# Kernel optimization log

Measured on AMD Instinct MI355X. Metric: run time of the kernel, lower is better.

## Reference

```python
import jax, jax.numpy as jnp
import numpy as np
from jax import lax

V, D, L = 32000, 1024, 8
HQ, HKV, HD = 16, 4, 64          # head_dim = D // HQ
H = int(2.6875 * D)              # SwiGLU hidden = 2752
B, S = 2, 1024
WINDOW, GEVERY = 256, 4
EPS, BASE = 1e-6, 10000.0
STD = 0.02


def setup_inputs() -> dict:
    key = jax.random.key(0)
    ks = jax.random.split(key, 10)
    return {
        "idx": jax.random.randint(ks[0], (B, S), 0, V, dtype=jnp.int32),
        "emb": jax.random.normal(ks[1], (V, D), jnp.float32) * STD,
        "Wq": jax.random.normal(ks[2], (L, D, HQ * HD), jnp.float32) * STD,
        "Wk": jax.random.normal(ks[3], (L, D, HKV * HD), jnp.float32) * STD,
        "Wv": jax.random.normal(ks[4], (L, D, HKV * HD), jnp.float32) * STD,
        "Wo": jax.random.normal(ks[5], (L, HQ * HD, D), jnp.float32) * (STD / np.sqrt(2 * L)).astype(np.float32),
        "w1": jax.random.normal(ks[6], (L, D, H), jnp.float32) * STD,
        "w3": jax.random.normal(ks[7], (L, D, H), jnp.float32) * STD,
        "w2": jax.random.normal(ks[8], (L, H, D), jnp.float32) * (STD / np.sqrt(2 * L)).astype(np.float32),
        "n1": jnp.ones((L, D), jnp.float32),
        "n2": jnp.ones((L, D), jnp.float32),
        "nf": jnp.ones((D,), jnp.float32),
    }


def _rmsnorm(x, w):
    return x * lax.rsqrt(jnp.mean(x * x, axis=-1, keepdims=True) + EPS) * w


def _rope(x, cos, sin):
    # x: [B,S,h,HD]; pairs (even, odd) rotated by complex multiply with e^{i*theta}
    x2 = x.reshape(*x.shape[:-1], HD // 2, 2)
    x0, x1 = x2[..., 0], x2[..., 1]
    r0 = x0 * cos - x1 * sin
    r1 = x0 * sin + x1 * cos
    return jnp.stack([r0, r1], axis=-1).reshape(x.shape)


def _forward(idx, emb, Wq, Wk, Wv, Wo, w1, w3, w2, n1, n2, nf):
    # RoPE cache (RoPECache._build_cache)
    inv_freq = 1.0 / (BASE ** (jnp.arange(0, HD, 2, dtype=jnp.float32) / HD))
    t = jnp.arange(S, dtype=jnp.float32)
    freqs = t[:, None] * inv_freq[None, :]                      # [S, HD//2]
    cos = jnp.cos(freqs)[None, :, None, :]                      # [1,S,1,HD//2]
    sin = jnp.sin(freqs)[None, :, None, :]

    # masks: global causal and sliding-window causal (additive, 0 / -inf)
    pos = jnp.arange(S)
    causal = pos[None, :] <= pos[:, None]
    local = causal & ((pos[:, None] - pos[None, :]) < WINDOW)
    neg_inf = jnp.float32(-jnp.inf)
    gmask = jnp.where(causal, 0.0, neg_inf).astype(jnp.float32)
    lmask = jnp.where(local, 0.0, neg_inf).astype(jnp.float32)
    use_global = ((jnp.arange(L) + 1) % GEVERY) == 0            # [L] bool

    scale = 1.0 / (HD ** 0.5)
    rep = HQ // HKV

    def block(x, p):
        wq, wk, wv, wo, W1, W3, W2, g1, g2, ug = p
        h = _rmsnorm(x, g1)
        q = (h @ wq).reshape(B, S, HQ, HD)
        k = (h @ wk).reshape(B, S, HKV, HD)
        v = (h @ wv).reshape(B, S, HKV, HD)
        q = _rope(q, cos, sin)
        k = _rope(k, cos, sin)
        k = jnp.repeat(k, rep, axis=2)                          # GQA: expand KV heads
        v = jnp.repeat(v, rep, axis=2)
        mask = jnp.where(ug, gmask, lmask)
        sc = jnp.einsum('bqhd,bkhd->bhqk', q, k) * scale + mask
        attn = jax.nn.softmax(sc, axis=-1)
        o = jnp.einsum('bhqk,bkhd->bqhd', attn, v).reshape(B, S, HQ * HD)
        x = x + o @ wo
        h2 = _rmsnorm(x, g2)
        x = x + (jax.nn.silu(h2 @ W1) * (h2 @ W3)) @ W2
        return x, None

    x = emb[idx]                                                # token embedding
    x, _ = lax.scan(block, x, (Wq, Wk, Wv, Wo, w1, w3, w2, n1, n2, use_global))
    logits = _rmsnorm(x, nf) @ emb.T                            # tied lm_head
    return logits


def reference(idx, emb, Wq, Wk, Wv, Wo, w1, w3, w2, n1, n2, nf):
    return _forward(idx, emb, Wq, Wk, Wv, Wo, w1, w3, w2, n1, n2, nf)
```

## Files before the change

### kernel.cpp

```cpp
#include <hip/hip_runtime.h>

#define V_ 32000
#define D_ 1024
#define L_ 8
#define HQ_ 16
#define HKV_ 4
#define HD_ 64
#define H_ 2752
#define B_ 2
#define S_ 1024
#define BS_ 2048
#define WINDOW_ 256

typedef float f32x4 __attribute__((ext_vector_type(4)));
typedef short s16x8 __attribute__((ext_vector_type(8)));
typedef unsigned short u16;

__device__ __forceinline__ u16 f2b(float f) {
  union { float f; unsigned u; } a; a.f = f;
  return (u16)((a.u + 0x7fffu + ((a.u >> 16) & 1u)) >> 16);
}
__device__ __forceinline__ float b2f(u16 b) {
  union { unsigned u; float f; } a; a.u = ((unsigned)b) << 16; return a.f;
}

__device__ __forceinline__ void gload_lds16(const void* g, void* l) {
  __builtin_amdgcn_global_load_lds(
      (const __attribute__((address_space(1))) void*)(unsigned long long)(uintptr_t)g,
      (__attribute__((address_space(3))) void*)(unsigned int)(uintptr_t)l,
      16, 0, 0);
}

__global__ void k_cvt(const float* __restrict__ src, u16* __restrict__ dst, long n4) {
  long i = (long)blockIdx.x * blockDim.x + threadIdx.x;
  if (i >= n4) return;
  float4 v = ((const float4*)src)[i];
  ushort4 o; o.x = f2b(v.x); o.y = f2b(v.y); o.z = f2b(v.z); o.w = f2b(v.w);
  ((ushort4*)dst)[i] = o;
}

struct TMat { const float* src; u16* dst; int R, C, t0, mul, add; };
struct T7 { TMat m[7]; };

__global__ void k_transpose7(T7 P) {
  __shared__ float tile[32][33];
  int bid = blockIdx.x;
  int mi = 0;
#pragma unroll
  for (int i = 1; i < 7; ++i) if (bid >= P.m[i].t0) mi = i;
  TMat mm = P.m[mi];
  int tl = bid - mm.t0;
  int ct = mm.C >> 5;
  int tr = tl / ct, tc = tl - tr * ct;
  int r0 = tr << 5, c0 = tc << 5;
  int tx = threadIdx.x & 31, ty = threadIdx.x >> 5;
#pragma unroll
  for (int j = 0; j < 4; ++j)
    tile[ty + j * 8][tx] = mm.src[(size_t)(r0 + ty + j * 8) * mm.C + c0 + tx];
  __syncthreads();
#pragma unroll
  for (int j = 0; j < 4; ++j)
    mm.dst[((size_t)(c0 + ty + j * 8) * mm.mul + mm.add) * mm.R + r0 + tx] =
        f2b(tile[tx][ty + j * 8]);
}

__global__ void k_embed(const int* __restrict__ idx, const float* __restrict__ emb,
                        float* __restrict__ x) {
  int t = blockIdx.x;
  int token = idx[t];
  const float4* s = (const float4*)(emb + (size_t)token * D_);
  float4* d = (float4*)(x + (size_t)t * D_);
  d[threadIdx.x] = s[threadIdx.x];
}

__global__ void k_rmsnorm(const float* __restrict__ x, const float* __restrict__ w,
                          u16* __restrict__ out) {
  int row = blockIdx.x, tid = threadIdx.x;
  float4 v = ((const float4*)(x + (size_t)row * D_))[tid];
  float ss = v.x * v.x + v.y * v.y + v.z * v.z + v.w * v.w;
#pragma unroll
  for (int m = 1; m < 64; m <<= 1) ss += __shfl_xor(ss, m, 64);
  __shared__ float red[4];
  if ((tid & 63) == 0) red[tid >> 6] = ss;
  __syncthreads();
  float tot = red[0] + red[1] + red[2] + red[3];
  float rs = rsqrtf(tot * (1.0f / D_) + 1e-6f);
  float4 wv = ((const float4*)w)[tid];
  ushort4 o;
  o.x = f2b(v.x * rs * wv.x); o.y = f2b(v.y * rs * wv.y);
  o.z = f2b(v.z * rs * wv.z); o.w = f2b(v.w * rs * wv.w);
  ((ushort4*)(out + (size_t)row * D_))[tid] = o;
}

__global__ void k_ropetab(float* __restrict__ cosT, float* __restrict__ sinT) {
  int i = blockIdx.x * blockDim.x + threadIdx.x;
  int s = i >> 5, d = i & 31;
  float inv = __expf(-((float)(2 * d) / (float)HD_) * logf(10000.0f));
  float f = (float)s * inv;
  cosT[i] = cosf(f); sinT[i] = sinf(f);
}

__global__ void k_ropev(const float* __restrict__ qkvf, const float* __restrict__ cosT,
                        const float* __restrict__ sinT, u16* __restrict__ qh,
                        u16* __restrict__ kh, u16* __restrict__ vth) {
  __shared__ float tile[32][65];
  int bid = blockIdx.x;
  int tid = threadIdx.x;
  if (bid < BS_) {
    int t = bid;
    int b = t >> 10, s = t & (S_ - 1);
    const float* row = qkvf + (size_t)t * 1536;
    for (int p = tid; p < 512; p += 256) {
      int hh = p >> 5, d = p & 31;
      float x0 = row[hh * 64 + 2 * d], x1 = row[hh * 64 + 2 * d + 1];
      float c = cosT[s * 32 + d], sn = sinT[s * 32 + d];
      size_t o = ((size_t)(b * HQ_ + hh) * S_ + s) * HD_ + 2 * d;
      qh[o] = f2b(x0 * c - x1 * sn);
      qh[o + 1] = f2b(x0 * sn + x1 * c);
    }
    if (tid < 128) {
      int hh = tid >> 5, d = tid & 31;
      float x0 = row[1024 + hh * 64 + 2 * d], x1 = row[1024 + hh * 64 + 2 * d + 1];
      float c = cosT[s * 32 + d], sn = sinT[s * 32 + d];
      size_t o = ((size_t)(b * HKV_ + hh) * S_ + s) * HD_ + 2 * d;
      kh[o] = f2b(x0 * c - x1 * sn);
      kh[o + 1] = f2b(x0 * sn + x1 * c);
    }
  } else {
    int v = bid - BS_;
    const int s0 = (v & 31) << 5, hh = (v >> 5) & 3, b = v >> 7;
    const int tx = tid & 63, ty = tid >> 6;
#pragma unroll
    for (int j = 0; j < 8; ++j) {
      int sl = j * 4 + ty;
      tile[sl][tx] = qkvf[(size_t)((b << 10) + s0 + sl) * 1536 + 1280 + hh * 64 + tx];
    }
    __syncthreads();
    const int sx = tid & 31, dr = tid >> 5;
#pragma unroll
    for (int j = 0; j < 8; ++j) {
      int d = j * 8 + dr;
      vth[((size_t)((b * HKV_ + hh) << 6) + d) * S_ + s0 + sx] = f2b(tile[sx][d]);
    }
  }
}

template <int EPI>
__global__ __launch_bounds__(256) void k_gemm(const u16* __restrict__ A,
                                              const u16* __restrict__ BT,
                                              void* __restrict__ Cp, int kdepth,
                                              int lda, int ldc) {
  __shared__ u16 As[3][4096];
  __shared__ u16 Bs[3][4096];
  const int tid = threadIdx.x;
  const int lane = tid & 63, wid = tid >> 6;
  const int lin = blockIdx.y * 16 + blockIdx.x;
  const int cpx = (gridDim.x * gridDim.y) >> 3;
  const int swz = (lin & 7) * cpx + (lin >> 3);
  const int m0 = (swz & 15) << 7, n0 = (swz >> 4) << 7;
  const int wm = (wid >> 1) << 6, wn = (wid & 1) << 6;
  const int fr = lane & 15, fg = lane >> 4;

  f32x4 acc[4][4] = {};

  const int srow = (wid << 4) + (lane >> 2);
  const int scol = ((lane & 3) - ((lane >> 3) & 3)) & 3;
  const int kz = blockIdx.z * kdepth;
  const u16* ga = A + (size_t)(m0 + srow) * lda + kz + (scol << 3);
  const u16* gb = BT + (size_t)(n0 + srow) * lda + kz + (scol << 3);
  const int cb = wid << 9;

  auto stage = [&](int buf, int k0) {
    u16* la = &As[buf][cb];
    u16* lb = &Bs[buf][cb];
    gload_lds16(ga + k0, la);
    gload_lds16(ga + (size_t)64 * lda + k0, la + 2048);
    gload_lds16(gb + k0, lb);
    gload_lds16(gb + (size_t)64 * lda + k0, lb + 2048);
  };

  const int nk = kdepth >> 5;
  stage(0, 0);
  stage(1, 32);

  const int ab = (wid >> 1) << 2, bb = (wid & 1) << 2;
  const int foff = (fr << 5) + ((((fg + (fr >> 1)) & 3)) << 3);
  int cur = 0;
  for (int t = 0; t < nk; ++t) {
    if (t + 2 < nk) {
      int nb = cur + 2; if (nb >= 3) nb -= 3;
      stage(nb, (t + 2) << 5);
      asm volatile("s_waitcnt vmcnt(8)" ::: "memory");
    } else if (t + 2 == nk) {
      asm volatile("s_waitcnt vmcnt(4)" ::: "memory");
    } else {
      asm volatile("s_waitcnt vmcnt(0)" ::: "memory");
    }
    __builtin_amdgcn_s_barrier();
    s16x8 af[4], bq[4];
#pragma unroll
    for (int i = 0; i < 4; ++i) {
      af[i] = *(const s16x8*)(&As[cur][((ab + i) << 9) + foff]);
      bq[i] = *(const s16x8*)(&Bs[cur][((bb + i) << 9) + foff]);
    }
#pragma unroll
    for (int mi = 0; mi < 4; ++mi)
#pragma unroll
      for (int ni = 0; ni < 4; ++ni)
        acc[mi][ni] = __builtin_amdgcn_mfma_f32_16x16x32_bf16(af[mi], bq[ni], acc[mi][ni], 0, 0, 0);
    __builtin_amdgcn_s_barrier();
    if (++cur == 3) cur = 0;
  }

#pragma unroll
  for (int mi = 0; mi < 4; ++mi) {
#pragma unroll
    for (int ni = 0; ni < 4; ++ni) {
#pragma unroll
      for (int r = 0; r < 4; ++r) {
        int row = m0 + wm + mi * 16 + fg * 4 + r;
        int col = n0 + wn + ni * 16 + fr;
        size_t off = (size_t)row * ldc + col;
        float v = acc[mi][ni][r];
        if (EPI == 0) ((float*)Cp)[off] = v;
        else atomicAdd((float*)Cp + off, v);
      }
    }
  }
}

template <int EPI>
__global__ __launch_bounds__(512, 4) void k_gemm2(const u16* __restrict__ A,
                                                  const u16* __restrict__ BT,
                                                  void* __restrict__ Cp, int K, int ldc) {
  __shared__ u16 As[3][8192];
  __shared__ u16 Bs[3][4096];
  const int tid = threadIdx.x;
  const int lane = tid & 63, wid = tid >> 6;
  const int lin = blockIdx.y * gridDim.x + blockIdx.x;
  const int cpx = (gridDim.x * gridDim.y) >> 3;
  const int swz = (lin & 7) * cpx + (lin >> 3);
  const int m0 = (swz & 7) << 8, n0 = (swz >> 3) << 7;
  const int fr = lane & 15, fg = lane >> 4;

  f32x4 acc[4][4] = {};

  const int srow = lane >> 2;
  const int scol = ((lane & 3) - ((lane >> 3) & 3)) & 3;
  const u16* ga = A + (size_t)(m0 + (wid << 5) + srow) * K + (scol << 3);
  const u16* gb = BT + (size_t)(n0 + (wid << 4) + srow) * K + (scol << 3);
  const int cba = wid << 10;
  const int cbb = wid << 9;

  auto stage = [&](int buf, int k0) {
    gload_lds16(ga + k0, &As[buf][cba]);
    gload_lds16(ga + (size_t)16 * K + k0, &As[buf][cba + 512]);
    gload_lds16(gb + k0, &Bs[buf][cbb]);
  };

  const int nk = K >> 5;
  stage(0, 0);
  stage(1, 32);

  const int am = (wid >> 1) << 2;
  const int bn = (wid & 1) << 2;
  const int foff = (fr << 5) + ((((fg + (fr >> 1)) & 3)) << 3);
  int cur = 0;
  for (int t = 0; t < nk; ++t) {
    if (t + 2 < nk) {
      int nb = cur + 2; if (nb >= 3) nb -= 3;
      stage(nb, (t + 2) << 5);
      asm volatile("s_waitcnt vmcnt(6)" ::: "memory");
    } else if (t + 2 == nk) {
      asm volatile("s_waitcnt vmcnt(3)" ::: "memory");
    } else {
      asm volatile("s_waitcnt vmcnt(0)" ::: "memory");
    }
    __builtin_amdgcn_s_barrier();
    s16x8 af[4], bq[4];
#pragma unroll
    for (int i = 0; i < 4; ++i) {
      af[i] = *(const s16x8*)(&As[cur][((am + i) << 9) + foff]);
      bq[i] = *(const s16x8*)(&Bs[cur][((bn + i) << 9) + foff]);
    }
#pragma unroll
    for (int mi = 0; mi < 4; ++mi)
#pragma unroll
      for (int ni = 0; ni < 4; ++ni)
        acc[mi][ni] = __builtin_amdgcn_mfma_f32_16x16x32_bf16(af[mi], bq[ni], acc[mi][ni], 0, 0, 0);
    __builtin_amdgcn_s_barrier();
    if (++cur == 3) cur = 0;
  }

#pragma unroll
  for (int mi = 0; mi < 4; ++mi) {
#pragma unroll
    for (int ni = 0; ni < 4; ++ni) {
#pragma unroll
      for (int r = 0; r < 4; ++r) {
        int row = m0 + ((wid >> 1) << 6) + mi * 16 + fg * 4 + r;
        int col = n0 + ((wid & 1) << 6) + ni * 16 + fr;
        float v = acc[mi][ni][r];
        if (EPI == 0) {
          ((float*)Cp)[(size_t)row * ldc + col] = v;
        } else {
          float o = __shfl_xor(v, 1, 64);
          if (!(fr & 1)) {
            float s = v / (1.0f + __expf(-v)) * o;
            ((u16*)Cp)[(size_t)row * ldc + (col >> 1)] = f2b(s);
          }
        }
      }
    }
  }
}

__global__ __launch_bounds__(256) void k_attn(const u16* __restrict__ qh,
                                              const u16* __restrict__ kh,
                                              const u16* __restrict__ vth,
                                              u16* __restrict__ attno, int isGlobal) {
  __shared__ u16 pb[4][512];
  const int qblk = blockIdx.x, hq = blockIdx.y, b = blockIdx.z;
  const int lane = threadIdx.x & 63, wid = threadIdx.x >> 6;
  const int fr = lane & 15, fg = lane >> 4;
  const int q0 = (qblk << 6) + (wid << 4);
  const int hk = hq >> 2;
  const u16* Q = qh + ((size_t)(b * HQ_ + hq) * S_) * HD_;
  const u16* Kh = kh + ((size_t)(b * HKV_ + hk) * S_) * HD_;
  const u16* VT = vth + ((size_t)(b * HKV_ + hk) * HD_) * S_;
  u16* pbuf = pb[wid];

  const s16x8 aq0 = *(const s16x8*)(Q + (q0 + fr) * HD_ + fg * 8);
  const s16x8 aq1 = *(const s16x8*)(Q + (q0 + fr) * HD_ + 32 + fg * 8);

  f32x4 o0 = {}, o1 = {}, o2 = {}, o3 = {};
  float m[4], l[4];
#pragma unroll
  for (int r = 0; r < 4; ++r) { m[r] = -1e30f; l[r] = 0.0f; }

  int kt0 = 0;
  if (!isGlobal) { int lo = q0 - (WINDOW_ - 1); if (lo > 0) kt0 = lo & ~31; }
  const int ktend = q0 + 16;

  for (int kt = kt0; kt < ktend; kt += 32) {
    f32x4 sc0 = {}, sc1 = {};
    {
      s16x8 b0 = *(const s16x8*)(Kh + (kt + fr) * HD_ + fg * 8);
      s16x8 b1 = *(const s16x8*)(Kh + (kt + fr) * HD_ + 32 + fg * 8);
      sc0 = __builtin_amdgcn_mfma_f32_16x16x32_bf16(aq0, b0, sc0, 0, 0, 0);
      sc0 = __builtin_amdgcn_mfma_f32_16x16x32_bf16(aq1, b1, sc0, 0, 0, 0);
      s16x8 c0 = *(const s16x8*)(Kh + (kt + 16 + fr) * HD_ + fg * 8);
      s16x8 c1 = *(const s16x8*)(Kh + (kt + 16 + fr) * HD_ + 32 + fg * 8);
      sc1 = __builtin_amdgcn_mfma_f32_16x16x32_bf16(aq0, c0, sc1, 0, 0, 0);
      sc1 = __builtin_amdgcn_mfma_f32_16x16x32_bf16(aq1, c1, sc1, 0, 0, 0);
    }
#pragma unroll
    for (int r = 0; r < 4; ++r) {
      int row = q0 + fg * 4 + r;
      int col0 = kt + fr, col1 = kt + 16 + fr;
      bool v0 = (col0 <= row) && (isGlobal || (row - col0) < WINDOW_);
      bool v1 = (col1 <= row) && (isGlobal || (row - col1) < WINDOW_);
      float s0 = v0 ? sc0[r] * 0.125f : -1e30f;
      float s1 = v1 ? sc1[r] * 0.125f : -1e30f;
      float t = fmaxf(s0, s1);
#pragma unroll
      for (int msk = 1; msk < 16; msk <<= 1) t = fmaxf(t, __shfl_xor(t, msk, 16));
      float mn = fmaxf(m[r], t);
      float fsc = __expf(m[r] - mn);
      m[r] = mn;
      float p0 = v0 ? __expf(s0 - mn) : 0.0f;
      float p1 = v1 ? __expf(s1 - mn) : 0.0f;
      float ps = p0 + p1;
#pragma unroll
      for (int msk = 1; msk < 16; msk <<= 1) ps += __shfl_xor(ps, msk, 16);
      l[r] = l[r] * fsc + ps;
      o0[r] *= fsc; o1[r] *= fsc; o2[r] *= fsc; o3[r] *= fsc;
      pbuf[(fg * 4 + r) * 32 + fr] = f2b(p0);
      pbuf[(fg * 4 + r) * 32 + 16 + fr] = f2b(p1);
    }
    s16x8 ap = *(const s16x8*)(pbuf + fr * 32 + fg * 8);
    {
      s16x8 bv0 = *(const s16x8*)(VT + (size_t)(0 + fr) * S_ + kt + fg * 8);
      o0 = __builtin_amdgcn_mfma_f32_16x16x32_bf16(ap, bv0, o0, 0, 0, 0);
      s16x8 bv1 = *(const s16x8*)(VT + (size_t)(16 + fr) * S_ + kt + fg * 8);
      o1 = __builtin_amdgcn_mfma_f32_16x16x32_bf16(ap, bv1, o1, 0, 0, 0);
      s16x8 bv2 = *(const s16x8*)(VT + (size_t)(32 + fr) * S_ + kt + fg * 8);
      o2 = __builtin_amdgcn_mfma_f32_16x16x32_bf16(ap, bv2, o2, 0, 0, 0);
      s16x8 bv3 = *(const s16x8*)(VT + (size_t)(48 + fr) * S_ + kt + fg * 8);
      o3 = __builtin_amdgcn_mfma_f32_16x16x32_bf16(ap, bv3, o3, 0, 0, 0);
    }
  }

#pragma unroll
  for (int r = 0; r < 4; ++r) {
    int row = q0 + fg * 4 + r;
    float inv = 1.0f / l[r];
    size_t base = ((size_t)b * S_ + row) * (HQ_ * HD_) + hq * HD_;
    attno[base + fr] = f2b(o0[r] * inv);
    attno[base + 16 + fr] = f2b(o1[r] * inv);
    attno[base + 32 + fr] = f2b(o2[r] * inv);
    attno[base + 48 + fr] = f2b(o3[r] * inv);
  }
}

extern "C" void kernel_launch(void* const* d_in, const int* in_sizes, int n_in,
                              void* d_out, int out_size, void* d_ws, size_t ws_size,
                              hipStream_t stream) {
  (void)in_sizes; (void)n_in; (void)out_size; (void)ws_size;
  const int* idx = (const int*)d_in[0];
  const float* emb = (const float*)d_in[1];
  const float* Wq = (const float*)d_in[2];
  const float* Wk = (const float*)d_in[3];
  const float* Wv = (const float*)d_in[4];
  const float* Wo = (const float*)d_in[5];
  const float* w1 = (const float*)d_in[6];
  const float* w3 = (const float*)d_in[7];
  const float* w2 = (const float*)d_in[8];
  const float* n1 = (const float*)d_in[9];
  const float* n2 = (const float*)d_in[10];
  const float* nf = (const float*)d_in[11];
  float* out = (float*)d_out;

  char* p = (char*)d_ws;
  auto carve = [&](size_t bytes) {
    char* q = p;
    p += (bytes + 255) & ~(size_t)255;
    return (void*)q;
  };
  float* x = (float*)carve((size_t)BS_ * D_ * 4);
  u16* h = (u16*)carve((size_t)BS_ * D_ * 2);
  float* qkvf = (float*)carve((size_t)BS_ * 1536 * 4);
  u16* qh = (u16*)carve((size_t)B_ * HQ_ * S_ * HD_ * 2);
  u16* khb = (u16*)carve((size_t)B_ * HKV_ * S_ * HD_ * 2);
  u16* vth = (u16*)carve((size_t)B_ * HKV_ * HD_ * S_ * 2);
  u16* attno = (u16*)carve((size_t)BS_ * D_ * 2);
  u16* g = (u16*)carve((size_t)BS_ * H_ * 2);
  u16* wT = (u16*)carve((size_t)11075584 * 2);
  float* cosT = (float*)carve((size_t)S_ * 32 * 4);
  float* sinT = (float*)carve((size_t)S_ * 32 * 4);
  u16* embb = (u16*)carve((size_t)V_ * D_ * 2);

  k_cvt<<<V_ * D_ / 4 / 256, 256, 0, stream>>>(emb, embb, (long)V_ * D_ / 4);
  k_ropetab<<<S_ * 32 / 256, 256, 0, stream>>>(cosT, sinT);
  k_embed<<<BS_, 256, 0, stream>>>(idx, emb, x);

  for (int l = 0; l < L_; ++l) {
    T7 t7;
    t7.m[0] = { Wq + (size_t)l * D_ * 1024, wT, D_, 1024, 0, 1, 0 };
    t7.m[1] = { Wk + (size_t)l * D_ * 256, wT + 1048576, D_, 256, 1024, 1, 0 };
    t7.m[2] = { Wv + (size_t)l * D_ * 256, wT + 1310720, D_, 256, 1280, 1, 0 };
    t7.m[3] = { Wo + (size_t)l * 1024 * D_, wT + 1572864, 1024, D_, 1536, 1, 0 };
    t7.m[4] = { w1 + (size_t)l * D_ * H_, wT + 2621440, D_, H_, 2560, 2, 0 };
    t7.m[5] = { w3 + (size_t)l * D_ * H_, wT + 2621440, D_, H_, 5312, 2, 1 };
    t7.m[6] = { w2 + (size_t)l * H_ * D_, wT + 8257536, H_, D_, 8064, 1, 0 };
    k_transpose7<<<10816, 256, 0, stream>>>(t7);

    k_rmsnorm<<<BS_, 256, 0, stream>>>(x, n1 + (size_t)l * D_, h);
    k_gemm<0><<<dim3(16, 12), 256, 0, stream>>>(h, wT, qkvf, 1024, 1024, 1536);
    k_ropev<<<BS_ + 256, 256, 0, stream>>>(qkvf, cosT, sinT, qh, khb, vth);
    int ig = ((l + 1) % 4) == 0;
    k_attn<<<dim3(16, HQ_, B_), 256, 0, stream>>>(qh, khb, vth, attno, ig);
    k_gemm<4><<<dim3(16, 8, 2), 256, 0, stream>>>(attno, wT + 1572864, x, 512, 1024, 1024);
    k_rmsnorm<<<BS_, 256, 0, stream>>>(x, n2 + (size_t)l * D_, h);
    k_gemm2<3><<<dim3(8, 43), 512, 0, stream>>>(h, wT + 2621440, g, 1024, 2752);
    k_gemm<4><<<dim3(16, 8, 2), 256, 0, stream>>>(g, wT + 8257536, x, 1376, 2752, 1024);
  }

  k_rmsnorm<<<BS_, 256, 0, stream>>>(x, nf, h);
  k_gemm2<0><<<dim3(8, 250), 512, 0, stream>>>(h, embb, out, 1024, 32000);
}
```

Measured before the change: 1.496 ms.

## Use 4-stage LDS ring with two K-steps per barrier in large GEMM

Turns the big GEMM kernel's triple-buffered LDS pipeline into a 4-buffer ring. Each iteration now prefetches and computes two K-slices, so there is one barrier pair per two K-steps instead of per step. It also raises wave priority around the MFMA blocks with s_setprio. The costs are more shared memory per block (96KB vs 72KB), which can reduce blocks per CU, and dropping the min-occupancy launch bound. The pipeline also assumes nk is even.

```diff
diff --git a/kernel.cpp b/kernel.cpp
--- a/kernel.cpp
+++ b/kernel.cpp
@@ -230,11 +230,11 @@
 }
 
 template <int EPI>
-__global__ __launch_bounds__(512, 4) void k_gemm2(const u16* __restrict__ A,
-                                                  const u16* __restrict__ BT,
-                                                  void* __restrict__ Cp, int K, int ldc) {
-  __shared__ u16 As[3][8192];
-  __shared__ u16 Bs[3][4096];
+__global__ __launch_bounds__(512) void k_gemm8(const u16* __restrict__ A,
+                                               const u16* __restrict__ BT,
+                                               void* __restrict__ Cp, int K, int ldc) {
+  __shared__ u16 As[4][8192];
+  __shared__ u16 Bs[4][4096];
   const int tid = threadIdx.x;
   const int lane = tid & 63, wid = tid >> 6;
   const int lin = blockIdx.y * gridDim.x + blockIdx.x;
@@ -265,31 +265,49 @@
   const int am = (wid >> 1) << 2;
   const int bn = (wid & 1) << 2;
   const int foff = (fr << 5) + ((((fg + (fr >> 1)) & 3)) << 3);
-  int cur = 0;
-  for (int t = 0; t < nk; ++t) {
-    if (t + 2 < nk) {
-      int nb = cur + 2; if (nb >= 3) nb -= 3;
-      stage(nb, (t + 2) << 5);
+  for (int j = 0; j < (nk >> 1); ++j) {
+    const int t0 = j << 1;
+    const int c0 = t0 & 3, c1 = (t0 + 1) & 3;
+    if (t0 + 2 < nk) {
+      stage((t0 + 2) & 3, (t0 + 2) << 5);
+      stage((t0 + 3) & 3, (t0 + 3) << 5);
       asm volatile("s_waitcnt vmcnt(6)" ::: "memory");
-    } else if (t + 2 == nk) {
-      asm volatile("s_waitcnt vmcnt(3)" ::: "memory");
     } else {
       asm volatile("s_waitcnt vmcnt(0)" ::: "memory");
     }
     __builtin_amdgcn_s_barrier();
-    s16x8 af[4], bq[4];
-#pragma unroll
-    for (int i = 0; i < 4; ++i) {
-      af[i] = *(const s16x8*)(&As[cur][((am + i) << 9) + foff]);
-      bq[i] = *(const s16x8*)(&Bs[cur][((bn + i) << 9) + foff]);
-    }
-#pragma unroll
-    for (int mi = 0; mi < 4; ++mi)
-#pragma unroll
-      for (int ni = 0; ni < 4; ++ni)
-        acc[mi][ni] = __builtin_amdgcn_mfma_f32_16x16x32_bf16(af[mi], bq[ni], acc[mi][ni], 0, 0, 0);
+    {
+      s16x8 af[4], bq[4];
+#pragma unroll
+      for (int i = 0; i < 4; ++i) {
+        af[i] = *(const s16x8*)(&As[c0][((am + i) << 9) + foff]);
+        bq[i] = *(const s16x8*)(&Bs[c0][((bn + i) << 9) + foff]);
+      }
+      __builtin_amdgcn_s_setprio(1);
+#pragma unroll
+      for (int mi = 0; mi < 4; ++mi)
+#pragma unroll
+        for (int ni = 0; ni < 4; ++ni)
+          acc[mi][ni] = __builtin_amdgcn_mfma_f32_16x16x32_bf16(af[mi], bq[ni], acc[mi][ni], 0, 0, 0);
+      __builtin_amdgcn_s_setprio(0);
+    }
+    {
+      s16x8 af[4], bq[4];
+#pragma unroll
+      for (int i = 0; i < 4; ++i) {
+        af[i] = *(const s16x8*)(&As[c1][((am + i) << 9) + foff]);
+        bq[i] = *(const s16x8*)(&Bs[c1][((bn + i) << 9) + foff]);
+      }
+      __builtin_amdgcn_s_setprio(1);
+#pragma unroll
+      for (int mi = 0; mi < 4; ++mi)
+#pragma unroll
+        for (int ni = 0; ni < 4; ++ni)
+          acc[mi][ni] = __builtin_amdgcn_mfma_f32_16x16x32_bf16(af[mi], bq[ni], acc[mi][ni], 0, 0, 0);
+      __builtin_amdgcn_s_setprio(0);
+    }
+    asm volatile("" ::: "memory");
     __builtin_amdgcn_s_barrier();
-    if (++cur == 3) cur = 0;
   }
 
 #pragma unroll
@@ -462,10 +480,10 @@
     k_attn<<<dim3(16, HQ_, B_), 256, 0, stream>>>(qh, khb, vth, attno, ig);
     k_gemm<4><<<dim3(16, 8, 2), 256, 0, stream>>>(attno, wT + 1572864, x, 512, 1024, 1024);
     k_rmsnorm<<<BS_, 256, 0, stream>>>(x, n2 + (size_t)l * D_, h);
-    k_gemm2<3><<<dim3(8, 43), 512, 0, stream>>>(h, wT + 2621440, g, 1024, 2752);
+    k_gemm8<3><<<dim3(8, 43), 512, 0, stream>>>(h, wT + 2621440, g, 1024, 2752);
     k_gemm<4><<<dim3(16, 8, 2), 256, 0, stream>>>(g, wT + 8257536, x, 1376, 2752, 1024);
   }
 
   k_rmsnorm<<<BS_, 256, 0, stream>>>(x, nf, h);
-  k_gemm2<0><<<dim3(8, 250), 512, 0, stream>>>(h, embb, out, 1024, 32000);
-}
+  k_gemm8<0><<<dim3(8, 250), 512, 0, stream>>>(h, embb, out, 1024, 32000);
+}
```

Result: slower. 1.667 ms (+11.5%).

## Fuse RoPE into QKV GEMM epilogue and merge init kernels

Applied to the files above, without the earlier changes.

Applies the rotary embedding to Q and K directly in the QKV GEMM epilogue, using a lane shuffle to fetch the paired even/odd element and writing bf16 head-major outputs. Only V is still written as fp32 and transposed by a slimmed kernel. The bf16 embedding conversion and RoPE table kernels are merged into one launch. This removes the fp32 round trip of Q/K through global memory and a few launches, at the cost of scattered 2-byte stores and table loads in the GEMM epilogue.

```diff
diff --git a/kernel.cpp b/kernel.cpp
--- a/kernel.cpp
+++ b/kernel.cpp
@@ -31,12 +31,21 @@
       16, 0, 0);
 }
 
-__global__ void k_cvt(const float* __restrict__ src, u16* __restrict__ dst, long n4) {
-  long i = (long)blockIdx.x * blockDim.x + threadIdx.x;
-  if (i >= n4) return;
-  float4 v = ((const float4*)src)[i];
-  ushort4 o; o.x = f2b(v.x); o.y = f2b(v.y); o.z = f2b(v.z); o.w = f2b(v.w);
-  ((ushort4*)dst)[i] = o;
+__global__ void k_init(const float* __restrict__ src, u16* __restrict__ dst,
+                       float* __restrict__ cosT, float* __restrict__ sinT) {
+  int bid = blockIdx.x;
+  if (bid < 32000) {
+    long i = (long)bid * 256 + threadIdx.x;
+    float4 v = ((const float4*)src)[i];
+    ushort4 o; o.x = f2b(v.x); o.y = f2b(v.y); o.z = f2b(v.z); o.w = f2b(v.w);
+    ((ushort4*)dst)[i] = o;
+  } else {
+    int i = (bid - 32000) * 256 + threadIdx.x;
+    int s = i >> 5, d = i & 31;
+    float inv = __expf(-((float)(2 * d) / (float)HD_) * logf(10000.0f));
+    float f = (float)s * inv;
+    cosT[i] = cosf(f); sinT[i] = sinf(f);
+  }
 }
 
 struct TMat { const float* src; u16* dst; int R, C, t0, mul, add; };
@@ -92,56 +101,21 @@
   ((ushort4*)(out + (size_t)row * D_))[tid] = o;
 }
 
-__global__ void k_ropetab(float* __restrict__ cosT, float* __restrict__ sinT) {
-  int i = blockIdx.x * blockDim.x + threadIdx.x;
-  int s = i >> 5, d = i & 31;
-  float inv = __expf(-((float)(2 * d) / (float)HD_) * logf(10000.0f));
-  float f = (float)s * inv;
-  cosT[i] = cosf(f); sinT[i] = sinf(f);
-}
-
-__global__ void k_ropev(const float* __restrict__ qkvf, const float* __restrict__ cosT,
-                        const float* __restrict__ sinT, u16* __restrict__ qh,
-                        u16* __restrict__ kh, u16* __restrict__ vth) {
+__global__ void k_vtrans(const float* __restrict__ qkvf, u16* __restrict__ vth) {
   __shared__ float tile[32][65];
-  int bid = blockIdx.x;
-  int tid = threadIdx.x;
-  if (bid < BS_) {
-    int t = bid;
-    int b = t >> 10, s = t & (S_ - 1);
-    const float* row = qkvf + (size_t)t * 1536;
-    for (int p = tid; p < 512; p += 256) {
-      int hh = p >> 5, d = p & 31;
-      float x0 = row[hh * 64 + 2 * d], x1 = row[hh * 64 + 2 * d + 1];
-      float c = cosT[s * 32 + d], sn = sinT[s * 32 + d];
-      size_t o = ((size_t)(b * HQ_ + hh) * S_ + s) * HD_ + 2 * d;
-      qh[o] = f2b(x0 * c - x1 * sn);
-      qh[o + 1] = f2b(x0 * sn + x1 * c);
-    }
-    if (tid < 128) {
-      int hh = tid >> 5, d = tid & 31;
-      float x0 = row[1024 + hh * 64 + 2 * d], x1 = row[1024 + hh * 64 + 2 * d + 1];
-      float c = cosT[s * 32 + d], sn = sinT[s * 32 + d];
-      size_t o = ((size_t)(b * HKV_ + hh) * S_ + s) * HD_ + 2 * d;
-      kh[o] = f2b(x0 * c - x1 * sn);
-      kh[o + 1] = f2b(x0 * sn + x1 * c);
-    }
-  } else {
-    int v = bid - BS_;
-    const int s0 = (v & 31) << 5, hh = (v >> 5) & 3, b = v >> 7;
-    const int tx = tid & 63, ty = tid >> 6;
-#pragma unroll
-    for (int j = 0; j < 8; ++j) {
-      int sl = j * 4 + ty;
-      tile[sl][tx] = qkvf[(size_t)((b << 10) + s0 + sl) * 1536 + 1280 + hh * 64 + tx];
-    }
-    __syncthreads();
-    const int sx = tid & 31, dr = tid >> 5;
-#pragma unroll
-    for (int j = 0; j < 8; ++j) {
-      int d = j * 8 + dr;
-      vth[((size_t)((b * HKV_ + hh) << 6) + d) * S_ + s0 + sx] = f2b(tile[sx][d]);
-    }
+  const int s0 = blockIdx.x << 5, hh = blockIdx.y, b = blockIdx.z;
+  const int tx = threadIdx.x & 63, ty = threadIdx.x >> 6;
+#pragma unroll
+  for (int j = 0; j < 8; ++j) {
+    int sl = j * 4 + ty;
+    tile[sl][tx] = qkvf[(size_t)((b << 10) + s0 + sl) * 1536 + 1280 + hh * 64 + tx];
+  }
+  __syncthreads();
+  const int sx = threadIdx.x & 31, dr = threadIdx.x >> 5;
+#pragma unroll
+  for (int j = 0; j < 8; ++j) {
+    int d = j * 8 + dr;
+    vth[((size_t)((b * HKV_ + hh) << 6) + d) * S_ + s0 + sx] = f2b(tile[sx][d]);
   }
 }
 
@@ -149,7 +123,11 @@
 __global__ __launch_bounds__(256) void k_gemm(const u16* __restrict__ A,
                                               const u16* __restrict__ BT,
                                               void* __restrict__ Cp, int kdepth,
-                                              int lda, int ldc) {
+                                              int lda, int ldc,
+                                              const float* __restrict__ cosT,
+                                              const float* __restrict__ sinT,
+                                              u16* __restrict__ qh,
+                                              u16* __restrict__ kh) {
   __shared__ u16 As[3][4096];
   __shared__ u16 Bs[3][4096];
   const int tid = threadIdx.x;
@@ -220,10 +198,29 @@
       for (int r = 0; r < 4; ++r) {
         int row = m0 + wm + mi * 16 + fg * 4 + r;
         int col = n0 + wn + ni * 16 + fr;
-        size_t off = (size_t)row * ldc + col;
         float v = acc[mi][ni][r];
-        if (EPI == 0) ((float*)Cp)[off] = v;
-        else atomicAdd((float*)Cp + off, v);
+        if (EPI == 0) {
+          ((float*)Cp)[(size_t)row * ldc + col] = v;
+        } else if (EPI == 4) {
+          atomicAdd((float*)Cp + (size_t)row * ldc + col, v);
+        } else {
+          float o = __shfl_xor(v, 1, 64);
+          int s = row & (S_ - 1), bb2 = row >> 10;
+          if (col < 1280) {
+            int d = (col & 63) >> 1;
+            float c = cosT[s * 32 + d], sn = sinT[s * 32 + d];
+            float res = (fr & 1) ? (o * sn + v * c) : (v * c - o * sn);
+            if (col < 1024) {
+              int hh = col >> 6;
+              qh[((size_t)(bb2 * HQ_ + hh) * S_ + s) * HD_ + (col & 63)] = f2b(res);
+            } else {
+              int hh = (col - 1024) >> 6;
+              kh[((size_t)(bb2 * HKV_ + hh) * S_ + s) * HD_ + (col & 63)] = f2b(res);
+            }
+          } else {
+            ((float*)Cp)[(size_t)row * ldc + col] = v;
+          }
+        }
       }
     }
   }
@@ -440,8 +437,7 @@
   float* sinT = (float*)carve((size_t)S_ * 32 * 4);
   u16* embb = (u16*)carve((size_t)V_ * D_ * 2);
 
-  k_cvt<<<V_ * D_ / 4 / 256, 256, 0, stream>>>(emb, embb, (long)V_ * D_ / 4);
-  k_ropetab<<<S_ * 32 / 256, 256, 0, stream>>>(cosT, sinT);
+  k_init<<<32128, 256, 0, stream>>>(emb, embb, cosT, sinT);
   k_embed<<<BS_, 256, 0, stream>>>(idx, emb, x);
 
   for (int l = 0; l < L_; ++l) {
@@ -456,14 +452,17 @@
     k_transpose7<<<10816, 256, 0, stream>>>(t7);
 
     k_rmsnorm<<<BS_, 256, 0, stream>>>(x, n1 + (size_t)l * D_, h);
-    k_gemm<0><<<dim3(16, 12), 256, 0, stream>>>(h, wT, qkvf, 1024, 1024, 1536);
-    k_ropev<<<BS_ + 256, 256, 0, stream>>>(qkvf, cosT, sinT, qh, khb, vth);
+    k_gemm<5><<<dim3(16, 12), 256, 0, stream>>>(h, wT, qkvf, 1024, 1024, 1536,
+                                                cosT, sinT, qh, khb);
+    k_vtrans<<<dim3(32, HKV_, B_), 256, 0, stream>>>(qkvf, vth);
     int ig = ((l + 1) % 4) == 0;
     k_attn<<<dim3(16, HQ_, B_), 256, 0, stream>>>(qh, khb, vth, attno, ig);
-    k_gemm<4><<<dim3(16, 8, 2), 256, 0, stream>>>(attno, wT + 1572864, x, 512, 1024, 1024);
+    k_gemm<4><<<dim3(16, 8, 2), 256, 0, stream>>>(attno, wT + 1572864, x, 512, 1024, 1024,
+                                                  nullptr, nullptr, nullptr, nullptr);
     k_rmsnorm<<<BS_, 256, 0, stream>>>(x, n2 + (size_t)l * D_, h);
     k_gemm2<3><<<dim3(8, 43), 512, 0, stream>>>(h, wT + 2621440, g, 1024, 2752);
-    k_gemm<4><<<dim3(16, 8, 2), 256, 0, stream>>>(g, wT + 8257536, x, 1376, 2752, 1024);
+    k_gemm<4><<<dim3(16, 8, 2), 256, 0, stream>>>(g, wT + 8257536, x, 1376, 2752, 1024,
+                                                  nullptr, nullptr, nullptr, nullptr);
   }
 
   k_rmsnorm<<<BS_, 256, 0, stream>>>(x, nf, h);
```

New measurement: 1.576 ms. 1.05x slower.
